# Performance work log

Hardware: AMD Instinct MI355X
Metric: run time of the kernel (lower is better)

The kernel has to match this reference:

```python
import jax, jax.numpy as jnp
import numpy as np

B, D, N_TYPES = 512, 768, 16
MARGIN = 1.0


def setup_inputs() -> dict:
    key = jax.random.key(0)
    k1, k2 = jax.random.split(key)
    entity_types = jax.random.randint(k1, (B,), 0, N_TYPES, dtype=jnp.int64)
    embeddings = jax.random.normal(k2, (B, D), dtype=jnp.float32)
    return {"entity_types": entity_types, "embeddings": embeddings}


def _pairwise_l2(x):
    # Euclidean distance matrix [B, B], matching torch.cdist(x, x, p=2)
    sq_norm = jnp.sum(x * x, axis=-1)  # [B]
    sq = sq_norm[:, None] + sq_norm[None, :] - 2.0 * (x @ x.T)
    sq = jnp.maximum(sq, 0.0)
    # safe sqrt: zero gradient where sq == 0 (diagonal)
    return jnp.where(sq > 0, jnp.sqrt(jnp.where(sq > 0, sq, 1.0)), 0.0)


def reference(entity_types, embeddings):
    # type_coherence[i, j] = (type_i == type_j)
    type_coherence = entity_types[:, None] == entity_types[None, :]  # [B, B]
    # valid_triplets[a, p, n] = same_type(a, p) & different_type(a, n)
    valid_triplets = type_coherence[:, :, None] & (~type_coherence)[:, None, :]  # [B, B, B]
    distances = _pairwise_l2(embeddings)  # [B, B]
    # triplet_distances[a, p, n] = (d[a, p] - d[a, n]) masked by validity
    triplet_distances = (distances[:, :, None] - distances[:, None, :]) * valid_triplets
    # NOTE: faithful to original — margin added to ALL B^3 entries before clamp,
    # so each invalid triplet contributes clamp(margin, 0) = margin to the sum.
    loss = jnp.sum(jnp.maximum(triplet_distances + MARGIN, 0.0))
    return loss / jnp.sum(valid_triplets)
```

## Files before the change

### kernel.cpp

```cpp
#include <hip/hip_runtime.h>
#include <hip/hip_bf16.h>

#define BSZ 512
#define DIM 768
#define KSPLIT 4
#define KSEG (DIM / KSPLIT)
#define TILE 64
#define NTYPES 16
#define MARGIN 1.0f
#define LDSPITCH (KSEG + 8)

typedef short bf16x8 __attribute__((ext_vector_type(8)));
typedef float f32x4 __attribute__((ext_vector_type(4)));

__global__ __launch_bounds__(256) void dot_partial_kernel(
    const float* __restrict__ emb,
    float* __restrict__ part,
    float* __restrict__ ndiag,
    float* __restrict__ out)
{
    const int tid = threadIdx.x;
    const int blk = blockIdx.x;
    const int ks = blk >> 6;
    const int tile = blk & 63;
    const int ti = tile >> 3, tj = tile & 7;
    const int i0 = ti * TILE, j0 = tj * TILE;

    if (blk == 0 && tid == 0) out[0] = 0.f;

    __shared__ ushort sA[TILE][LDSPITCH];
    __shared__ ushort sB[TILE][LDSPITCH];

    #pragma unroll
    for (int it = 0; it < 24; ++it) {
        const int flat = it * 256 + tid;
        const int row = flat / 48;
        const int c4 = flat - row * 48;
        const int grow = (row < TILE) ? (i0 + row) : (j0 + row - TILE);
        const float4 v = *(const float4*)(emb + (size_t)grow * DIM + ks * KSEG + c4 * 4);
        __hip_bfloat162 h0 = __float22bfloat162_rn(make_float2(v.x, v.y));
        __hip_bfloat162 h1 = __float22bfloat162_rn(make_float2(v.z, v.w));
        unsigned u0, u1;
        __builtin_memcpy(&u0, &h0, 4);
        __builtin_memcpy(&u1, &h1, 4);
        ushort* dst = (row < TILE) ? &sA[row][c4 * 4] : &sB[row - TILE][c4 * 4];
        *(uint2*)dst = make_uint2(u0, u1);
    }
    __syncthreads();

    const int lane = tid & 63;
    const int w = tid >> 6;
    const int m = lane & 15;
    const int q = lane >> 4;

    f32x4 acc0 = {0.f, 0.f, 0.f, 0.f};
    f32x4 acc1 = {0.f, 0.f, 0.f, 0.f};
    f32x4 acc2 = {0.f, 0.f, 0.f, 0.f};
    f32x4 acc3 = {0.f, 0.f, 0.f, 0.f};

    const ushort* arow = &sA[w * 16 + m][q * 8];
    const ushort* b0r = &sB[0 * 16 + m][q * 8];
    const ushort* b1r = &sB[1 * 16 + m][q * 8];
    const ushort* b2r = &sB[2 * 16 + m][q * 8];
    const ushort* b3r = &sB[3 * 16 + m][q * 8];

    #pragma unroll
    for (int kc = 0; kc < KSEG / 32; ++kc) {
        const bf16x8 af = *(const bf16x8*)(arow + kc * 32);
        const bf16x8 bf0 = *(const bf16x8*)(b0r + kc * 32);
        const bf16x8 bf1 = *(const bf16x8*)(b1r + kc * 32);
        const bf16x8 bf2 = *(const bf16x8*)(b2r + kc * 32);
        const bf16x8 bf3 = *(const bf16x8*)(b3r + kc * 32);
        acc0 = __builtin_amdgcn_mfma_f32_16x16x32_bf16(af, bf0, acc0, 0, 0, 0);
        acc1 = __builtin_amdgcn_mfma_f32_16x16x32_bf16(af, bf1, acc1, 0, 0, 0);
        acc2 = __builtin_amdgcn_mfma_f32_16x16x32_bf16(af, bf2, acc2, 0, 0, 0);
        acc3 = __builtin_amdgcn_mfma_f32_16x16x32_bf16(af, bf3, acc3, 0, 0, 0);
    }

    float* pbuf = part + (size_t)ks * BSZ * BSZ;
    const int gi = i0 + w * 16 + 4 * q;
    #pragma unroll
    for (int r = 0; r < 4; ++r) {
        float* prow = pbuf + (size_t)(gi + r) * BSZ + j0;
        prow[0 * 16 + m] = acc0[r];
        prow[1 * 16 + m] = acc1[r];
        prow[2 * 16 + m] = acc2[r];
        prow[3 * 16 + m] = acc3[r];
    }
    if (ti == tj && (m >> 2) == q) {
        const f32x4 accw = (w == 0) ? acc0 : (w == 1) ? acc1 : (w == 2) ? acc2 : acc3;
        ndiag[ks * BSZ + i0 + w * 16 + m] = accw[m & 3];
    }
}

__global__ __launch_bounds__(256) void triplet_kernel(
    const float* __restrict__ part, const float* __restrict__ ndiag,
    const int* __restrict__ types, float* __restrict__ out)
{
    const int a = blockIdx.x;
    const int tid = threadIdx.x;
    const int lane = tid & 63;
    __shared__ float nrm[BSZ];
    __shared__ float pos[BSZ], neg[BSZ];
    __shared__ int npos, nneg;
    __shared__ float wsum[4];
    __shared__ int cnt[NTYPES];
    if (tid == 0) { npos = 0; nneg = 0; }
    if (tid < NTYPES) cnt[tid] = 0;
    for (int j = tid; j < BSZ; j += 256)
        nrm[j] = ndiag[j] + ndiag[BSZ + j] + ndiag[2 * BSZ + j] + ndiag[3 * BSZ + j];
    const int ta = types[a];
    __syncthreads();

    const float na = nrm[a];
    const size_t rb = (size_t)a * BSZ;
    const size_t PS = (size_t)BSZ * BSZ;

    for (int j = tid; j < BSZ; j += 256) {
        const int tj = types[j];
        atomicAdd(&cnt[tj], 1);
        const float sp = part[rb + j] + part[PS + rb + j]
                       + part[2 * PS + rb + j] + part[3 * PS + rb + j];
        const float d = sqrtf(fmaxf(na + nrm[j] - 2.f * sp, 0.f));
        const bool isp = (tj == ta);
        const unsigned long long mm = __ballot(isp);
        const unsigned long long below = mm & ((1ull << lane) - 1ull);
        const int cp = __popcll(mm);
        int basep = 0, basen = 0;
        if (lane == 0) {
            basep = atomicAdd(&npos, cp);
            basen = atomicAdd(&nneg, 64 - cp);
        }
        basep = __shfl(basep, 0);
        basen = __shfl(basen, 0);
        const int pbelow = (int)__popcll(below);
        if (isp) pos[basep + pbelow] = d;
        else     neg[basen + (lane - pbelow)] = d;
    }
    __syncthreads();
    const int np = npos, nn = nneg;

    float local = 0.f;
    for (int pi = 0; pi < np; ++pi) {
        const float dpm = pos[pi] + MARGIN;
        for (int n = tid; n < nn; n += 256)
            local += fmaxf(dpm - neg[n], 0.f);
    }

    #pragma unroll
    for (int off = 32; off > 0; off >>= 1) local += __shfl_down(local, off);
    if (lane == 0) wsum[tid >> 6] = local;
    __syncthreads();
    if (tid == 0) {
        long long V = 0;
        #pragma unroll
        for (int t = 0; t < NTYPES; ++t) {
            long long c = cnt[t];
            V += c * c * (long long)(BSZ - c);
        }
        double blocksum = (double)wsum[0] + (double)wsum[1]
                        + (double)wsum[2] + (double)wsum[3];
        float contrib = (float)(blocksum / (double)V);
        if (a == 0) {
            const long long B3 = (long long)BSZ * BSZ * BSZ;
            contrib += (float)((double)(B3 - V) * (double)MARGIN / (double)V);
        }
        atomicAdd(out, contrib);
    }
}

extern "C" void kernel_launch(void* const* d_in, const int* in_sizes, int n_in,
                              void* d_out, int out_size, void* d_ws, size_t ws_size,
                              hipStream_t stream) {
    const int* types = (const int*)d_in[0];
    const float* emb = (const float*)d_in[1];
    float* out = (float*)d_out;

    float* part = (float*)d_ws;
    float* ndiag = part + (size_t)KSPLIT * BSZ * BSZ;

    dot_partial_kernel<<<256, 256, 0, stream>>>(emb, part, ndiag, out);
    triplet_kernel<<<BSZ, 256, 0, stream>>>(part, ndiag, types, out);
}
```

Baseline: 73.49 us.

## Fuse distance GEMM and triplet reduction into one per-anchor-group kernel

Replaces the split-K dot-product kernel and the separate triplet kernel with a single kernel. Each of 32 blocks handles 16 anchors and computes their distances to all 512 embeddings with MFMA, double-buffering the B operand in LDS and computing norms on the fly. Distances stay in LDS and the pos/neg partition and hinge sum run in the same block, so the 4 MB partial-product workspace round trip and the second launch go away. In exchange every block re-reads the whole embedding matrix, only 32 blocks occupy the GPU, and the output reset now races with atomic adds from other blocks of the same launch.

```diff
diff --git a/kernel.cpp b/kernel.cpp
--- a/kernel.cpp
+++ b/kernel.cpp
@@ -3,153 +3,166 @@
 
 #define BSZ 512
 #define DIM 768
-#define KSPLIT 4
-#define KSEG (DIM / KSPLIT)
-#define TILE 64
 #define NTYPES 16
 #define MARGIN 1.0f
-#define LDSPITCH (KSEG + 8)
+#define NANCH 16
+#define NBLK (BSZ / NANCH)
+#define KSEG 32
+#define NSEG (DIM / KSEG)
+#define BPITCH 40
+#define APITCH 776
+#define DPITCH 514
 
 typedef short bf16x8 __attribute__((ext_vector_type(8)));
 typedef float f32x4 __attribute__((ext_vector_type(4)));
 
-__global__ __launch_bounds__(256) void dot_partial_kernel(
+__global__ __launch_bounds__(256) void fused_triplet_kernel(
     const float* __restrict__ emb,
-    float* __restrict__ part,
-    float* __restrict__ ndiag,
+    const int* __restrict__ types,
     float* __restrict__ out)
 {
     const int tid = threadIdx.x;
-    const int blk = blockIdx.x;
-    const int ks = blk >> 6;
-    const int tile = blk & 63;
-    const int ti = tile >> 3, tj = tile & 7;
-    const int i0 = ti * TILE, j0 = tj * TILE;
+    const int b = blockIdx.x;
 
-    if (blk == 0 && tid == 0) out[0] = 0.f;
+    if (b == 0 && tid == 0) atomicExch(out, 0.0f);
 
-    __shared__ ushort sA[TILE][LDSPITCH];
-    __shared__ ushort sB[TILE][LDSPITCH];
+    __shared__ ushort sB[2][BSZ][BPITCH];
+    __shared__ ushort sA[NANCH][APITCH];
+    __shared__ float dst[NANCH][DPITCH];
+    __shared__ float nrm[BSZ];
+    __shared__ float na[NANCH];
+    __shared__ float pos[BSZ], neg[BSZ];
+    __shared__ int   stypes[BSZ];
+    __shared__ int   cnt[NTYPES];
+    __shared__ int   npA[NANCH], nnA[NANCH];
+    __shared__ float wsum[4];
 
-    #pragma unroll
-    for (int it = 0; it < 24; ++it) {
-        const int flat = it * 256 + tid;
-        const int row = flat / 48;
-        const int c4 = flat - row * 48;
-        const int grow = (row < TILE) ? (i0 + row) : (j0 + row - TILE);
-        const float4 v = *(const float4*)(emb + (size_t)grow * DIM + ks * KSEG + c4 * 4);
-        __hip_bfloat162 h0 = __float22bfloat162_rn(make_float2(v.x, v.y));
-        __hip_bfloat162 h1 = __float22bfloat162_rn(make_float2(v.z, v.w));
-        unsigned u0, u1;
-        __builtin_memcpy(&u0, &h0, 4);
-        __builtin_memcpy(&u1, &h1, 4);
-        ushort* dst = (row < TILE) ? &sA[row][c4 * 4] : &sB[row - TILE][c4 * 4];
-        *(uint2*)dst = make_uint2(u0, u1);
+    {
+        const int row = tid >> 4;
+        const int c0 = tid & 15;
+        const float* src = emb + (size_t)(b * NANCH + row) * DIM;
+        float qn = 0.f;
+        #pragma unroll
+        for (int i = 0; i < 12; ++i) {
+            const int c4 = c0 + 16 * i;
+            const float4 v = *(const float4*)(src + c4 * 4);
+            qn += v.x * v.x + v.y * v.y + v.z * v.z + v.w * v.w;
+            __hip_bfloat162 h0 = __float22bfloat162_rn(make_float2(v.x, v.y));
+            __hip_bfloat162 h1 = __float22bfloat162_rn(make_float2(v.z, v.w));
+            unsigned u0, u1;
+            __builtin_memcpy(&u0, &h0, 4);
+            __builtin_memcpy(&u1, &h1, 4);
+            *(uint2*)&sA[row][c4 * 4] = make_uint2(u0, u1);
+        }
+        qn += __shfl_xor(qn, 1); qn += __shfl_xor(qn, 2);
+        qn += __shfl_xor(qn, 4); qn += __shfl_xor(qn, 8);
+        if (c0 == 0) na[row] = qn;
     }
-    __syncthreads();
+    if (tid < NTYPES) cnt[tid] = 0;
+    if (tid < NANCH) { npA[tid] = 0; nnA[tid] = 0; }
+    for (int j = tid; j < BSZ; j += 256) stypes[j] = types[j];
+
+    auto stageB = [&](int s, int buf) {
+        const int rsub = tid >> 2;
+        const int c0 = tid & 3;
+        #pragma unroll
+        for (int p = 0; p < 8; ++p) {
+            const int row = p * 64 + rsub;
+            const float* src = emb + (size_t)row * DIM + s * KSEG;
+            float qn = 0.f;
+            #pragma unroll
+            for (int i = 0; i < 2; ++i) {
+                const int c4 = c0 + 4 * i;
+                const float4 v = *(const float4*)(src + c4 * 4);
+                qn += v.x * v.x + v.y * v.y + v.z * v.z + v.w * v.w;
+                __hip_bfloat162 h0 = __float22bfloat162_rn(make_float2(v.x, v.y));
+                __hip_bfloat162 h1 = __float22bfloat162_rn(make_float2(v.z, v.w));
+                unsigned u0, u1;
+                __builtin_memcpy(&u0, &h0, 4);
+                __builtin_memcpy(&u1, &h1, 4);
+                *(uint2*)&sB[buf][row][c4 * 4] = make_uint2(u0, u1);
+            }
+            qn += __shfl_xor(qn, 1); qn += __shfl_xor(qn, 2);
+            if (c0 == 0) nrm[row] = (s == 0) ? qn : (nrm[row] + qn);
+        }
+    };
 
     const int lane = tid & 63;
     const int w = tid >> 6;
     const int m = lane & 15;
-    const int q = lane >> 4;
+    const int qq = lane >> 4;
 
-    f32x4 acc0 = {0.f, 0.f, 0.f, 0.f};
-    f32x4 acc1 = {0.f, 0.f, 0.f, 0.f};
-    f32x4 acc2 = {0.f, 0.f, 0.f, 0.f};
-    f32x4 acc3 = {0.f, 0.f, 0.f, 0.f};
+    f32x4 acc[8];
+    #pragma unroll
+    for (int t = 0; t < 8; ++t) acc[t] = (f32x4){0.f, 0.f, 0.f, 0.f};
 
-    const ushort* arow = &sA[w * 16 + m][q * 8];
-    const ushort* b0r = &sB[0 * 16 + m][q * 8];
-    const ushort* b1r = &sB[1 * 16 + m][q * 8];
-    const ushort* b2r = &sB[2 * 16 + m][q * 8];
-    const ushort* b3r = &sB[3 * 16 + m][q * 8];
+    stageB(0, 0);
+    __syncthreads();
+
+    #pragma unroll 2
+    for (int s = 0; s < NSEG; ++s) {
+        if (s + 1 < NSEG) stageB(s + 1, (s + 1) & 1);
+        {
+            const ushort* ap = &sA[m][s * KSEG + qq * 8];
+            const bf16x8 af = *(const bf16x8*)ap;
+            const ushort* bp = &sB[s & 1][w * 128 + m][qq * 8];
+            #pragma unroll
+            for (int t = 0; t < 8; ++t) {
+                const bf16x8 bf = *(const bf16x8*)(bp + t * 16 * BPITCH);
+                acc[t] = __builtin_amdgcn_mfma_f32_16x16x32_bf16(af, bf, acc[t], 0, 0, 0);
+            }
+        }
+        __syncthreads();
+    }
 
     #pragma unroll
-    for (int kc = 0; kc < KSEG / 32; ++kc) {
-        const bf16x8 af = *(const bf16x8*)(arow + kc * 32);
-        const bf16x8 bf0 = *(const bf16x8*)(b0r + kc * 32);
-        const bf16x8 bf1 = *(const bf16x8*)(b1r + kc * 32);
-        const bf16x8 bf2 = *(const bf16x8*)(b2r + kc * 32);
-        const bf16x8 bf3 = *(const bf16x8*)(b3r + kc * 32);
-        acc0 = __builtin_amdgcn_mfma_f32_16x16x32_bf16(af, bf0, acc0, 0, 0, 0);
-        acc1 = __builtin_amdgcn_mfma_f32_16x16x32_bf16(af, bf1, acc1, 0, 0, 0);
-        acc2 = __builtin_amdgcn_mfma_f32_16x16x32_bf16(af, bf2, acc2, 0, 0, 0);
-        acc3 = __builtin_amdgcn_mfma_f32_16x16x32_bf16(af, bf3, acc3, 0, 0, 0);
+    for (int t = 0; t < 8; ++t) {
+        const int j = w * 128 + t * 16 + m;
+        const float nj = nrm[j];
+        #pragma unroll
+        for (int r = 0; r < 4; ++r) {
+            const int ar = 4 * qq + r;
+            const float sq = na[ar] + nj - 2.f * acc[t][r];
+            dst[ar][j] = sqrtf(fmaxf(sq, 0.f));
+        }
     }
-
-    float* pbuf = part + (size_t)ks * BSZ * BSZ;
-    const int gi = i0 + w * 16 + 4 * q;
-    #pragma unroll
-    for (int r = 0; r < 4; ++r) {
-        float* prow = pbuf + (size_t)(gi + r) * BSZ + j0;
-        prow[0 * 16 + m] = acc0[r];
-        prow[1 * 16 + m] = acc1[r];
-        prow[2 * 16 + m] = acc2[r];
-        prow[3 * 16 + m] = acc3[r];
-    }
-    if (ti == tj && (m >> 2) == q) {
-        const f32x4 accw = (w == 0) ? acc0 : (w == 1) ? acc1 : (w == 2) ? acc2 : acc3;
-        ndiag[ks * BSZ + i0 + w * 16 + m] = accw[m & 3];
-    }
-}
-
-__global__ __launch_bounds__(256) void triplet_kernel(
-    const float* __restrict__ part, const float* __restrict__ ndiag,
-    const int* __restrict__ types, float* __restrict__ out)
-{
-    const int a = blockIdx.x;
-    const int tid = threadIdx.x;
-    const int lane = tid & 63;
-    __shared__ float nrm[BSZ];
-    __shared__ float pos[BSZ], neg[BSZ];
-    __shared__ int npos, nneg;
-    __shared__ float wsum[4];
-    __shared__ int cnt[NTYPES];
-    if (tid == 0) { npos = 0; nneg = 0; }
-    if (tid < NTYPES) cnt[tid] = 0;
-    for (int j = tid; j < BSZ; j += 256)
-        nrm[j] = ndiag[j] + ndiag[BSZ + j] + ndiag[2 * BSZ + j] + ndiag[3 * BSZ + j];
-    const int ta = types[a];
-    __syncthreads();
-
-    const float na = nrm[a];
-    const size_t rb = (size_t)a * BSZ;
-    const size_t PS = (size_t)BSZ * BSZ;
-
-    for (int j = tid; j < BSZ; j += 256) {
-        const int tj = types[j];
-        atomicAdd(&cnt[tj], 1);
-        const float sp = part[rb + j] + part[PS + rb + j]
-                       + part[2 * PS + rb + j] + part[3 * PS + rb + j];
-        const float d = sqrtf(fmaxf(na + nrm[j] - 2.f * sp, 0.f));
-        const bool isp = (tj == ta);
-        const unsigned long long mm = __ballot(isp);
-        const unsigned long long below = mm & ((1ull << lane) - 1ull);
-        const int cp = __popcll(mm);
-        int basep = 0, basen = 0;
-        if (lane == 0) {
-            basep = atomicAdd(&npos, cp);
-            basen = atomicAdd(&nneg, 64 - cp);
-        }
-        basep = __shfl(basep, 0);
-        basen = __shfl(basen, 0);
-        const int pbelow = (int)__popcll(below);
-        if (isp) pos[basep + pbelow] = d;
-        else     neg[basen + (lane - pbelow)] = d;
-    }
-    __syncthreads();
-    const int np = npos, nn = nneg;
+    for (int j = tid; j < BSZ; j += 256) atomicAdd(&cnt[stypes[j]], 1);
 
     float local = 0.f;
-    for (int pi = 0; pi < np; ++pi) {
-        const float dpm = pos[pi] + MARGIN;
-        for (int n = tid; n < nn; n += 256)
-            local += fmaxf(dpm - neg[n], 0.f);
+    for (int a = 0; a < NANCH; ++a) {
+        __syncthreads();
+        const int ta = stypes[b * NANCH + a];
+        #pragma unroll
+        for (int jj = 0; jj < 2; ++jj) {
+            const int j = jj * 256 + tid;
+            const float d = dst[a][j];
+            const bool isp = (stypes[j] == ta);
+            const unsigned long long mm = __ballot(isp);
+            const unsigned long long below = mm & ((1ull << lane) - 1ull);
+            const int cp = __popcll(mm);
+            int basep = 0, basen = 0;
+            if (lane == 0) {
+                basep = atomicAdd(&npA[a], cp);
+                basen = atomicAdd(&nnA[a], 64 - cp);
+            }
+            basep = __shfl(basep, 0);
+            basen = __shfl(basen, 0);
+            const int pb = (int)__popcll(below);
+            if (isp) pos[basep + pb] = d;
+            else     neg[basen + (lane - pb)] = d;
+        }
+        __syncthreads();
+        const int np = npA[a], nn = nnA[a];
+        for (int pi = w; pi < np; pi += 4) {
+            const float dpm = pos[pi] + MARGIN;
+            for (int n = lane; n < nn; n += 64)
+                local += fmaxf(dpm - neg[n], 0.f);
+        }
     }
 
     #pragma unroll
     for (int off = 32; off > 0; off >>= 1) local += __shfl_down(local, off);
-    if (lane == 0) wsum[tid >> 6] = local;
+    if (lane == 0) wsum[w] = local;
     __syncthreads();
     if (tid == 0) {
         long long V = 0;
@@ -158,10 +171,9 @@
             long long c = cnt[t];
             V += c * c * (long long)(BSZ - c);
         }
-        double blocksum = (double)wsum[0] + (double)wsum[1]
-                        + (double)wsum[2] + (double)wsum[3];
-        float contrib = (float)(blocksum / (double)V);
-        if (a == 0) {
+        double bs = (double)wsum[0] + (double)wsum[1] + (double)wsum[2] + (double)wsum[3];
+        float contrib = (float)(bs / (double)V);
+        if (b == 0) {
             const long long B3 = (long long)BSZ * BSZ * BSZ;
             contrib += (float)((double)(B3 - V) * (double)MARGIN / (double)V);
         }
@@ -175,10 +187,6 @@
     const int* types = (const int*)d_in[0];
     const float* emb = (const float*)d_in[1];
     float* out = (float*)d_out;
-
-    float* part = (float*)d_ws;
-    float* ndiag = part + (size_t)KSPLIT * BSZ * BSZ;
-
-    dot_partial_kernel<<<256, 256, 0, stream>>>(emb, part, ndiag, out);
-    triplet_kernel<<<BSZ, 256, 0, stream>>>(part, ndiag, types, out);
+    (void)d_ws; (void)ws_size;
+    fused_triplet_kernel<<<NBLK, 256, 0, stream>>>(emb, types, out);
 }
```

Measured after the change: 209.6 us. 185% more time.

## Drop K-split Gram partials, use 32x32 full-K tiles, register-cache negatives

Applied to the files above, without the earlier changes.

The Gram kernel now computes each 32x32 output tile over the full 768-long K dimension instead of writing four K-split partial matrices. This removes the 4x partial write and the re-read traffic in the triplet kernel, at the cost of larger LDS staging per block and a longer serial MFMA chain, which is split into two accumulators. The triplet kernel keeps the negative distances in registers, padded with a large sentinel, and spreads positives across waves so that inner-loop LDS reads go away. It also stages types and norms in shared memory.

```diff
diff --git a/kernel.cpp b/kernel.cpp
--- a/kernel.cpp
+++ b/kernel.cpp
@@ -3,126 +3,108 @@
 
 #define BSZ 512
 #define DIM 768
-#define KSPLIT 4
-#define KSEG (DIM / KSPLIT)
-#define TILE 64
 #define NTYPES 16
 #define MARGIN 1.0f
-#define LDSPITCH (KSEG + 8)
+#define PITCH 776
 
 typedef short bf16x8 __attribute__((ext_vector_type(8)));
 typedef float f32x4 __attribute__((ext_vector_type(4)));
 
-__global__ __launch_bounds__(256) void dot_partial_kernel(
+
+__global__ __launch_bounds__(256) void gram_kernel(
     const float* __restrict__ emb,
-    float* __restrict__ part,
-    float* __restrict__ ndiag,
+    float* __restrict__ G,
+    float* __restrict__ nrm,
     float* __restrict__ out)
 {
     const int tid = threadIdx.x;
     const int blk = blockIdx.x;
-    const int ks = blk >> 6;
-    const int tile = blk & 63;
-    const int ti = tile >> 3, tj = tile & 7;
-    const int i0 = ti * TILE, j0 = tj * TILE;
+    const int ti = blk >> 4, tj = blk & 15;
+    const int i0 = ti * 32, j0 = tj * 32;
 
     if (blk == 0 && tid == 0) out[0] = 0.f;
 
-    __shared__ ushort sA[TILE][LDSPITCH];
-    __shared__ ushort sB[TILE][LDSPITCH];
+    __shared__ ushort sR[64][PITCH];
 
-    #pragma unroll
-    for (int it = 0; it < 24; ++it) {
+    #pragma unroll 12
+    for (int it = 0; it < 48; ++it) {
         const int flat = it * 256 + tid;
-        const int row = flat / 48;
-        const int c4 = flat - row * 48;
-        const int grow = (row < TILE) ? (i0 + row) : (j0 + row - TILE);
-        const float4 v = *(const float4*)(emb + (size_t)grow * DIM + ks * KSEG + c4 * 4);
+        const int row = flat / 192;
+        const int c4 = flat - row * 192;
+        const int grow = (row < 32) ? (i0 + row) : (j0 + row - 32);
+        const float4 v = *(const float4*)(emb + (size_t)grow * DIM + c4 * 4);
         __hip_bfloat162 h0 = __float22bfloat162_rn(make_float2(v.x, v.y));
         __hip_bfloat162 h1 = __float22bfloat162_rn(make_float2(v.z, v.w));
         unsigned u0, u1;
         __builtin_memcpy(&u0, &h0, 4);
         __builtin_memcpy(&u1, &h1, 4);
-        ushort* dst = (row < TILE) ? &sA[row][c4 * 4] : &sB[row - TILE][c4 * 4];
-        *(uint2*)dst = make_uint2(u0, u1);
+        *(uint2*)&sR[row][c4 * 4] = make_uint2(u0, u1);
     }
     __syncthreads();
 
     const int lane = tid & 63;
     const int w = tid >> 6;
+    const int wr = w >> 1, wc = w & 1;
     const int m = lane & 15;
     const int q = lane >> 4;
 
-    f32x4 acc0 = {0.f, 0.f, 0.f, 0.f};
-    f32x4 acc1 = {0.f, 0.f, 0.f, 0.f};
-    f32x4 acc2 = {0.f, 0.f, 0.f, 0.f};
-    f32x4 acc3 = {0.f, 0.f, 0.f, 0.f};
+    const ushort* arow = &sR[wr * 16 + m][q * 8];
+    const ushort* brow = &sR[32 + wc * 16 + m][q * 8];
 
-    const ushort* arow = &sA[w * 16 + m][q * 8];
-    const ushort* b0r = &sB[0 * 16 + m][q * 8];
-    const ushort* b1r = &sB[1 * 16 + m][q * 8];
-    const ushort* b2r = &sB[2 * 16 + m][q * 8];
-    const ushort* b3r = &sB[3 * 16 + m][q * 8];
-
+    f32x4 acc_e = {0.f, 0.f, 0.f, 0.f};
+    f32x4 acc_o = {0.f, 0.f, 0.f, 0.f};
     #pragma unroll
-    for (int kc = 0; kc < KSEG / 32; ++kc) {
-        const bf16x8 af = *(const bf16x8*)(arow + kc * 32);
-        const bf16x8 bf0 = *(const bf16x8*)(b0r + kc * 32);
-        const bf16x8 bf1 = *(const bf16x8*)(b1r + kc * 32);
-        const bf16x8 bf2 = *(const bf16x8*)(b2r + kc * 32);
-        const bf16x8 bf3 = *(const bf16x8*)(b3r + kc * 32);
-        acc0 = __builtin_amdgcn_mfma_f32_16x16x32_bf16(af, bf0, acc0, 0, 0, 0);
-        acc1 = __builtin_amdgcn_mfma_f32_16x16x32_bf16(af, bf1, acc1, 0, 0, 0);
-        acc2 = __builtin_amdgcn_mfma_f32_16x16x32_bf16(af, bf2, acc2, 0, 0, 0);
-        acc3 = __builtin_amdgcn_mfma_f32_16x16x32_bf16(af, bf3, acc3, 0, 0, 0);
+    for (int kc = 0; kc < 24; kc += 2) {
+        const bf16x8 ae = *(const bf16x8*)(arow + kc * 32);
+        const bf16x8 be = *(const bf16x8*)(brow + kc * 32);
+        const bf16x8 ao = *(const bf16x8*)(arow + kc * 32 + 32);
+        const bf16x8 bo = *(const bf16x8*)(brow + kc * 32 + 32);
+        acc_e = __builtin_amdgcn_mfma_f32_16x16x32_bf16(ae, be, acc_e, 0, 0, 0);
+        acc_o = __builtin_amdgcn_mfma_f32_16x16x32_bf16(ao, bo, acc_o, 0, 0, 0);
     }
 
-    float* pbuf = part + (size_t)ks * BSZ * BSZ;
-    const int gi = i0 + w * 16 + 4 * q;
+    const int gi = i0 + wr * 16 + 4 * q;
+    const int gj = j0 + wc * 16 + m;
+    float res[4];
     #pragma unroll
     for (int r = 0; r < 4; ++r) {
-        float* prow = pbuf + (size_t)(gi + r) * BSZ + j0;
-        prow[0 * 16 + m] = acc0[r];
-        prow[1 * 16 + m] = acc1[r];
-        prow[2 * 16 + m] = acc2[r];
-        prow[3 * 16 + m] = acc3[r];
+        res[r] = acc_e[r] + acc_o[r];
+        G[(size_t)(gi + r) * BSZ + gj] = res[r];
     }
-    if (ti == tj && (m >> 2) == q) {
-        const f32x4 accw = (w == 0) ? acc0 : (w == 1) ? acc1 : (w == 2) ? acc2 : acc3;
-        ndiag[ks * BSZ + i0 + w * 16 + m] = accw[m & 3];
-    }
+    if (ti == tj && wr == wc && (m >> 2) == q)
+        nrm[i0 + wr * 16 + m] = res[m & 3];
 }
 
 __global__ __launch_bounds__(256) void triplet_kernel(
-    const float* __restrict__ part, const float* __restrict__ ndiag,
+    const float* __restrict__ G, const float* __restrict__ nrm,
     const int* __restrict__ types, float* __restrict__ out)
 {
     const int a = blockIdx.x;
     const int tid = threadIdx.x;
     const int lane = tid & 63;
-    __shared__ float nrm[BSZ];
+    const int w = tid >> 6;
+
+    __shared__ float snrm[BSZ];
+    __shared__ int   stypes[BSZ];
     __shared__ float pos[BSZ], neg[BSZ];
-    __shared__ int npos, nneg;
+    __shared__ int   npos, nneg, cnt[NTYPES];
     __shared__ float wsum[4];
-    __shared__ int cnt[NTYPES];
+
     if (tid == 0) { npos = 0; nneg = 0; }
     if (tid < NTYPES) cnt[tid] = 0;
-    for (int j = tid; j < BSZ; j += 256)
-        nrm[j] = ndiag[j] + ndiag[BSZ + j] + ndiag[2 * BSZ + j] + ndiag[3 * BSZ + j];
-    const int ta = types[a];
+    for (int j = tid; j < BSZ; j += 256) { stypes[j] = types[j]; snrm[j] = nrm[j]; }
     __syncthreads();
 
-    const float na = nrm[a];
-    const size_t rb = (size_t)a * BSZ;
-    const size_t PS = (size_t)BSZ * BSZ;
+    const int ta = stypes[a];
+    const float na = snrm[a];
+    for (int j = tid; j < BSZ; j += 256) atomicAdd(&cnt[stypes[j]], 1);
 
-    for (int j = tid; j < BSZ; j += 256) {
-        const int tj = types[j];
-        atomicAdd(&cnt[tj], 1);
-        const float sp = part[rb + j] + part[PS + rb + j]
-                       + part[2 * PS + rb + j] + part[3 * PS + rb + j];
-        const float d = sqrtf(fmaxf(na + nrm[j] - 2.f * sp, 0.f));
-        const bool isp = (tj == ta);
+    #pragma unroll
+    for (int jj = 0; jj < 2; ++jj) {
+        const int j = jj * 256 + tid;
+        const float g = G[(size_t)a * BSZ + j];
+        const float d = sqrtf(fmaxf(na + snrm[j] - 2.f * g, 0.f));
+        const bool isp = (stypes[j] == ta);
         const unsigned long long mm = __ballot(isp);
         const unsigned long long below = mm & ((1ull << lane) - 1ull);
         const int cp = __popcll(mm);
@@ -133,23 +115,30 @@
         }
         basep = __shfl(basep, 0);
         basen = __shfl(basen, 0);
-        const int pbelow = (int)__popcll(below);
-        if (isp) pos[basep + pbelow] = d;
-        else     neg[basen + (lane - pbelow)] = d;
+        const int pb = (int)__popcll(below);
+        if (isp) pos[basep + pb] = d;
+        else     neg[basen + (lane - pb)] = d;
     }
     __syncthreads();
     const int np = npos, nn = nneg;
 
+    float nr[8];
+    #pragma unroll
+    for (int c = 0; c < 8; ++c) {
+        const int n = c * 64 + lane;
+        nr[c] = (n < nn) ? neg[n] : 3.0e38f;
+    }
     float local = 0.f;
-    for (int pi = 0; pi < np; ++pi) {
+    for (int pi = w; pi < np; pi += 4) {
         const float dpm = pos[pi] + MARGIN;
-        for (int n = tid; n < nn; n += 256)
-            local += fmaxf(dpm - neg[n], 0.f);
+        #pragma unroll
+        for (int c = 0; c < 8; ++c)
+            local += fmaxf(dpm - nr[c], 0.f);
     }
 
     #pragma unroll
     for (int off = 32; off > 0; off >>= 1) local += __shfl_down(local, off);
-    if (lane == 0) wsum[tid >> 6] = local;
+    if (lane == 0) wsum[w] = local;
     __syncthreads();
     if (tid == 0) {
         long long V = 0;
@@ -158,9 +147,9 @@
             long long c = cnt[t];
             V += c * c * (long long)(BSZ - c);
         }
-        double blocksum = (double)wsum[0] + (double)wsum[1]
-                        + (double)wsum[2] + (double)wsum[3];
-        float contrib = (float)(blocksum / (double)V);
+        double bs = (double)wsum[0] + (double)wsum[1]
+                  + (double)wsum[2] + (double)wsum[3];
+        float contrib = (float)(bs / (double)V);
         if (a == 0) {
             const long long B3 = (long long)BSZ * BSZ * BSZ;
             contrib += (float)((double)(B3 - V) * (double)MARGIN / (double)V);
@@ -176,9 +165,9 @@
     const float* emb = (const float*)d_in[1];
     float* out = (float*)d_out;
 
-    float* part = (float*)d_ws;
-    float* ndiag = part + (size_t)KSPLIT * BSZ * BSZ;
+    float* G = (float*)d_ws;
+    float* nrm = G + (size_t)BSZ * BSZ;
 
-    dot_partial_kernel<<<256, 256, 0, stream>>>(emb, part, ndiag, out);
-    triplet_kernel<<<BSZ, 256, 0, stream>>>(part, ndiag, types, out);
+    gram_kernel<<<256, 256, 0, stream>>>(emb, G, nrm, out);
+    triplet_kernel<<<BSZ, 256, 0, stream>>>(G, nrm, types, out);
 }
```

After: 71.07 us. 3.3% less time.
